# Kernel optimization log

Measured on AMD Instinct MI355X. Metric: run time of the kernel, lower is better.

## Reference

```python
import jax, jax.numpy as jnp
import numpy as np
import math, itertools


def _dct_consts():
    t = np.zeros((8, 8, 8, 8), dtype=np.float32)
    for x, y, u, v in itertools.product(range(8), repeat=4):
        t[x, y, u, v] = math.cos((2 * x + 1) * u * math.pi / 16) * math.cos((2 * y + 1) * v * math.pi / 16)
    alpha = np.array([1.0 / np.sqrt(2)] + [1.0] * 7, dtype=np.float32)
    scale = np.outer(alpha, alpha).astype(np.float32) * 0.25
    return jnp.asarray(t), jnp.asarray(scale)

_TENSOR, _SCALE = _dct_consts()


def setup_inputs() -> dict:
    key = jax.random.key(0)
    # 64 RGB 512x512 images unfolded into 8x8 blocks: [B, C, n_blocks, 8, 8]
    image = jax.random.uniform(key, (64, 3, 4096, 8, 8), dtype=jnp.float32) * 255.0
    return {"image": image}


def reference(image) -> jnp.ndarray:
    x = image - 128.0
    # tensordot(image, tensor, dims=2): contract last two spatial dims (x,y)
    # with basis -> frequency dims (u,v); then elementwise scale.
    out = _SCALE * jnp.einsum('...xy,xyuv->...uv', x, _TENSOR)
    return out.reshape(image.shape)
```

## Files before the change

### kernel.cpp

```cpp
#include <hip/hip_runtime.h>

typedef float fx4 __attribute__((ext_vector_type(4)));

__device__ __forceinline__ void dct8(const float a[8], float o[8]) {
    const float s0 = a[0] + a[7], s1 = a[1] + a[6], s2 = a[2] + a[5], s3 = a[3] + a[4];
    const float d0 = a[0] - a[7], d1 = a[1] - a[6], d2 = a[2] - a[5], d3 = a[3] - a[4];
    const float ss0 = s0 + s3, ss1 = s1 + s2;
    const float ds0 = s0 - s3, ds1 = s1 - s2;
    o[0] = ss0 + ss1;
    o[4] = 0.70710678f * (ss0 - ss1);
    o[2] = fmaf(0.92387953f, ds0,  0.38268343f * ds1);
    o[6] = fmaf(0.38268343f, ds0, -0.92387953f * ds1);
    o[1] = fmaf(0.98078528f, d0, fmaf( 0.83146961f, d1, fmaf( 0.55557023f, d2,  0.19509032f * d3)));
    o[3] = fmaf(0.83146961f, d0, fmaf(-0.19509032f, d1, fmaf(-0.98078528f, d2, -0.55557023f * d3)));
    o[5] = fmaf(0.55557023f, d0, fmaf(-0.98078528f, d1, fmaf( 0.19509032f, d2,  0.83146961f * d3)));
    o[7] = fmaf(0.19509032f, d0, fmaf(-0.55557023f, d1, fmaf( 0.83146961f, d2, -0.98078528f * d3)));
}

__global__ __launch_bounds__(256) void dct8x8_kernel(const float* __restrict__ in,
                                                     float* __restrict__ out,
                                                     int nthreads) {
    __shared__ float lds[256 * 9];

    int tid = blockIdx.x * 256 + threadIdx.x;
    if (tid >= nthreads) tid = nthreads - 1;
    const int lane = threadIdx.x;
    const int c = lane & 7;
    const size_t blk = (size_t)(tid >> 3);

    const float* bp = in + blk * 64 + c;
    float a[8];
#pragma unroll
    for (int x = 0; x < 8; ++x) a[x] = bp[x * 8];

    float B[8];
    dct8(a, B);
    B[0] -= 1024.0f;

#pragma unroll
    for (int u = 0; u < 8; ++u) lds[lane * 9 + u] = B[u];
    __syncthreads();

    const int gbase = (lane & ~7) * 9;
    float t[8];
#pragma unroll
    for (int y = 0; y < 8; ++y) t[y] = lds[gbase + y * 9 + c];

    float o[8];
    dct8(t, o);

    const float su = (c == 0) ? 0.35355339059f : 0.5f;
#pragma unroll
    for (int v = 0; v < 8; ++v) o[v] *= su * ((v == 0) ? 0.35355339059f : 0.5f);

    fx4 q0 = { o[0], o[1], o[2], o[3] };
    fx4 q1 = { o[4], o[5], o[6], o[7] };
    fx4* qp = reinterpret_cast<fx4*>(out) + (size_t)tid * 2;
    __builtin_nontemporal_store(q0, qp);
    __builtin_nontemporal_store(q1, qp + 1);
}

extern "C" void kernel_launch(void* const* d_in, const int* in_sizes, int n_in,
                              void* d_out, int out_size, void* d_ws, size_t ws_size,
                              hipStream_t stream) {
    const float* in = (const float*)d_in[0];
    float* out = (float*)d_out;
    const int n = in_sizes[0];
    const int nthreads = n / 8;
    const int grid = (nthreads + 255) / 256;
    hipLaunchKernelGGL(dct8x8_kernel, dim3(grid), dim3(256), 0, stream,
                       in, out, nthreads);
}
```

Baseline: 85.31 us.

## Replace LDS transpose with shuffle-based register transposes and vectorized loads

```diff
diff --git a/kernel.cpp b/kernel.cpp
--- a/kernel.cpp
+++ b/kernel.cpp
@@ -17,47 +17,54 @@
     o[7] = fmaf(0.19509032f, d0, fmaf(-0.55557023f, d1, fmaf( 0.83146961f, d2, -0.98078528f * d3)));
 }
 
+__device__ __forceinline__ void transpose8(float r[8], int lane) {
+#pragma unroll
+    for (int s = 0; s < 3; ++s) {
+        const int m = 1 << s;
+        const bool bit = (lane & m) != 0;
+#pragma unroll
+        for (int j0 = 0; j0 < 8; ++j0) {
+            if ((j0 & m) == 0) {
+                const int j1 = j0 | m;
+                float send = bit ? r[j0] : r[j1];
+                float recv = __shfl_xor(send, m, 8);
+                r[j0] = bit ? recv : r[j0];
+                r[j1] = bit ? r[j1] : recv;
+            }
+        }
+    }
+}
+
 __global__ __launch_bounds__(256) void dct8x8_kernel(const float* __restrict__ in,
-                                                     float* __restrict__ out,
-                                                     int nthreads) {
-    __shared__ float lds[256 * 9];
+                                                     float* __restrict__ out) {
+    const int tid = blockIdx.x * 256 + threadIdx.x;
+    const int l = threadIdx.x & 7;
 
-    int tid = blockIdx.x * 256 + threadIdx.x;
-    if (tid >= nthreads) tid = nthreads - 1;
-    const int lane = threadIdx.x;
-    const int c = lane & 7;
-    const size_t blk = (size_t)(tid >> 3);
+    const fx4* p = reinterpret_cast<const fx4*>(in) + (size_t)tid * 2;
+    fx4 v0 = p[0];
+    fx4 v1 = p[1];
+    float a[8] = { v0[0], v0[1], v0[2], v0[3], v1[0], v1[1], v1[2], v1[3] };
 
-    const float* bp = in + blk * 64 + c;
-    float a[8];
-#pragma unroll
-    for (int x = 0; x < 8; ++x) a[x] = bp[x * 8];
+    float r[8];
+    dct8(a, r);
+    r[0] -= 1024.0f;
 
-    float B[8];
-    dct8(a, B);
-    B[0] -= 1024.0f;
-
-#pragma unroll
-    for (int u = 0; u < 8; ++u) lds[lane * 9 + u] = B[u];
-    __syncthreads();
-
-    const int gbase = (lane & ~7) * 9;
-    float t[8];
-#pragma unroll
-    for (int y = 0; y < 8; ++y) t[y] = lds[gbase + y * 9 + c];
+    transpose8(r, l);
 
     float o[8];
-    dct8(t, o);
+    dct8(r, o);
 
-    const float su = (c == 0) ? 0.35355339059f : 0.5f;
+    const float sl = (l == 0) ? 0.35355339059f : 0.5f;
 #pragma unroll
-    for (int v = 0; v < 8; ++v) o[v] *= su * ((v == 0) ? 0.35355339059f : 0.5f);
+    for (int u = 0; u < 8; ++u) o[u] *= sl * ((u == 0) ? 0.35355339059f : 0.5f);
+
+    transpose8(o, l);
 
     fx4 q0 = { o[0], o[1], o[2], o[3] };
     fx4 q1 = { o[4], o[5], o[6], o[7] };
     fx4* qp = reinterpret_cast<fx4*>(out) + (size_t)tid * 2;
-    __builtin_nontemporal_store(q0, qp);
-    __builtin_nontemporal_store(q1, qp + 1);
+    qp[0] = q0;
+    qp[1] = q1;
 }
 
 extern "C" void kernel_launch(void* const* d_in, const int* in_sizes, int n_in,
@@ -69,5 +76,5 @@
     const int nthreads = n / 8;
     const int grid = (nthreads + 255) / 256;
     hipLaunchKernelGGL(dct8x8_kernel, dim3(grid), dim3(256), 0, stream,
-                       in, out, nthreads);
+                       in, out);
 }
```

Measured after the change: 88.84 us. 4.1% more time.
